# Kernel optimization log

Measured on AMD Instinct MI355X. Metric: run time of the kernel, lower is better.

Reference implementation:

```python
import jax, jax.numpy as jnp
import numpy as np

TOP_K = 8


def setup_inputs() -> dict:
    key = jax.random.key(0)
    ks = jax.random.split(key, 5)
    T, H, I, E = 4096, 2048, 1024, 64
    s = 0.02
    return {
        "x": jax.random.normal(ks[0], (T, H), jnp.float32),
        "gate_w": jax.random.normal(ks[1], (E, H), jnp.float32) * s,
        "gate_b": jax.random.normal(ks[2], (E,), jnp.float32) * s,
        "fc1_w": jax.random.normal(ks[3], (E, 2 * I, H), jnp.float32) * s,
        "fc2_w": jax.random.normal(ks[4], (E, H, I), jnp.float32) * s,
    }


def reference(x, gate_w, gate_b, fc1_w, fc2_w):
    # Router: [T, E] logits, top-k, softmax over selected logits in fp32.
    E = gate_w.shape[0]
    logits = x @ gate_w.T + gate_b
    topk_logits, topk_idx = jax.lax.top_k(logits, TOP_K)
    w = jax.nn.softmax(topk_logits.astype(jnp.float32), axis=-1).astype(x.dtype)
    # Per-token combine weight for each expert: [T, E] (0 if expert not selected).
    comb = (jax.nn.one_hot(topk_idx, E, dtype=x.dtype) * w[..., None]).sum(axis=1)
    # Scan over experts: each step is one dense GEMM-GeGLU-GEMM with masked combine.
    def body(acc, ew):
        W1, W2, c = ew  # W1 [2I, H], W2 [H, I], c [T]
        h_full = x @ W1.T                       # [T, 2I]
        h, g = jnp.split(h_full, 2, axis=-1)
        a = jax.nn.gelu(h, approximate=False) * (g + 1.0)  # custom GeGLU
        y = a @ W2.T                            # [T, H]
        return acc + c[:, None] * y, None

    out0 = jnp.zeros_like(x)
    out, _ = jax.lax.scan(body, out0, (fc1_w, fc2_w, comb.T))
    return out
```

## Files before the change

kernel.cpp:

```cpp
#include <hip/hip_runtime.h>
#include <hip/hip_bf16.h>
#include <cfloat>
#include <math.h>

#define T_TOK 4096
#define H_DIM 2048
#define E_NUM 64
#define I_DIM 1024
#define TOPK  8
#define BM    128
#define BK    64
#define MAXTILE 320

typedef __attribute__((ext_vector_type(4))) float f32x4;
typedef __attribute__((ext_vector_type(8))) short bf16x8;
typedef __attribute__((ext_vector_type(4))) int   i32x4;

__device__ __forceinline__ unsigned short f2bf(float f) {
    union { float f; unsigned int u; } v; v.f = f;
    unsigned int r = v.u + 0x7FFFu + ((v.u >> 16) & 1u);
    return (unsigned short)(r >> 16);
}
__device__ __forceinline__ unsigned int pack2(float a, float b) {
    return (unsigned int)f2bf(a) | ((unsigned int)f2bf(b) << 16);
}
__device__ __forceinline__ int cvtpk(float lo, float hi) {
    int r; asm("v_cvt_pk_bf16_f32 %0, %1, %2" : "=v"(r) : "v"(lo), "v"(hi)); return r;
}
__device__ __forceinline__ void gload16(const void* g, void* l) {
    __builtin_amdgcn_global_load_lds((const __attribute__((address_space(1))) unsigned int*)g,
                                     (__attribute__((address_space(3))) unsigned int*)l, 16, 0, 0);
}

__global__ __launch_bounds__(256)
void router_kernel(const float* __restrict__ x, const float* __restrict__ gw,
                   const float* __restrict__ gb, unsigned short* __restrict__ xb,
                   int* __restrict__ topk_idx, float* __restrict__ topk_w,
                   int* __restrict__ counts)
{
    const int t = blockIdx.x;
    const int tid = threadIdx.x;
    __shared__ float xs[H_DIM];
    __shared__ float logits[E_NUM];
    const float* xrow = x + (size_t)t * H_DIM;

    #pragma unroll
    for (int i = 0; i < 2; ++i) {
        int c = i * 1024 + tid * 4;
        f32x4 v = *(const f32x4*)(xrow + c);
        *(f32x4*)(xs + c) = v;
        uint2 pk; pk.x = pack2(v.x, v.y); pk.y = pack2(v.z, v.w);
        *(uint2*)(xb + (size_t)t * H_DIM + c) = pk;
    }
    __syncthreads();

    const int wave = tid >> 6, lane = tid & 63;
    for (int ee = 0; ee < 16; ++ee) {
        const int e = wave * 16 + ee;
        const float* g = gw + (size_t)e * H_DIM;
        float p = 0.f;
        #pragma unroll
        for (int i = 0; i < 8; ++i) {
            int c = (i * 64 + lane) * 4;
            f32x4 gv = *(const f32x4*)(g + c);
            f32x4 xv = *(const f32x4*)(xs + c);
            p += gv.x * xv.x + gv.y * xv.y + gv.z * xv.z + gv.w * xv.w;
        }
        #pragma unroll
        for (int s = 32; s > 0; s >>= 1) p += __shfl_xor(p, s, 64);
        if (lane == 0) logits[e] = p + gb[e];
    }
    __syncthreads();

    if (tid < 64) {
        float cur = logits[tid];
        float wv[TOPK]; int wi[TOPK];
        #pragma unroll
        for (int k = 0; k < TOPK; ++k) {
            float bv = cur; int bi = tid;
            #pragma unroll
            for (int s = 32; s > 0; s >>= 1) {
                float ov = __shfl_xor(bv, s, 64);
                int   oi = __shfl_xor(bi, s, 64);
                if (ov > bv || (ov == bv && oi < bi)) { bv = ov; bi = oi; }
            }
            wv[k] = bv; wi[k] = bi;
            if (tid == bi) cur = -FLT_MAX;
        }
        if (tid == 0) {
            float mx = wv[0], sum = 0.f, ex[TOPK];
            #pragma unroll
            for (int k = 0; k < TOPK; ++k) { ex[k] = expf(wv[k] - mx); sum += ex[k]; }
            #pragma unroll
            for (int k = 0; k < TOPK; ++k) {
                topk_idx[t * TOPK + k] = wi[k];
                topk_w[t * TOPK + k]   = ex[k] / sum;
                atomicAdd(&counts[wi[k]], 1);
            }
        }
    }
}

__global__ void scan_kernel(const int* __restrict__ counts, int* __restrict__ offsets,
                            int* __restrict__ cursors, int* __restrict__ tiles,
                            int* __restrict__ ntiles)
{
    if (threadIdx.x == 0) {
        int acc = 0, nt = 0;
        for (int e = 0; e < E_NUM; ++e) {
            offsets[e] = acc; cursors[e] = acc;
            int c = counts[e];
            for (int m = 0; m * BM < c; ++m) tiles[nt++] = (e << 16) | m;
            acc += c;
        }
        *ntiles = nt;
    }
}

__global__ void assign_kernel(const int* __restrict__ topk_idx, const float* __restrict__ topk_w,
                              int* __restrict__ cursors, int* __restrict__ tok_of,
                              float* __restrict__ w_of)
{
    int i = blockIdx.x * 256 + threadIdx.x;
    if (i >= T_TOK * TOPK) return;
    int e = topk_idx[i];
    int pos = atomicAdd(&cursors[e], 1);
    tok_of[pos] = i >> 3;
    w_of[pos]   = topk_w[i];
}

__global__ __launch_bounds__(256, 2)
void gemm1_kernel(const unsigned short* __restrict__ xb, const float* __restrict__ fc1,
                  const int* __restrict__ counts, const int* __restrict__ offsets,
                  const int* __restrict__ tok_of, const int* __restrict__ tiles,
                  const int* __restrict__ ntiles, unsigned short* __restrict__ a_all)
{
    const int ty = blockIdx.y;
    if (ty >= *ntiles) return;
    const int code = tiles[ty];
    const int e = code >> 16, m0 = (code & 0xffff) * BM;
    const int cnt = counts[e], off = offsets[e];
    const int n0 = blockIdx.x * BM;
    const float* W = fc1 + (size_t)e * (size_t)(2 * I_DIM) * H_DIM;

    __shared__ unsigned short sA[2][BM * BK];
    __shared__ unsigned short sB[2 * BM * BK];
    __shared__ int sTok[BM];

    const int tid = threadIdx.x;
    if (tid < BM) {
        int m = m0 + tid;
        sTok[tid] = tok_of[off + (m < cnt ? m : cnt - 1)];
    }
    __syncthreads();

    const int wid = tid >> 6, lane = tid & 63;
    const int srow = tid >> 3, sch = tid & 7;
    const int sslot = sch ^ (srow & 7);

    const unsigned short* aSrc[4];
    const float* bSrc[8];
    #pragma unroll
    for (int i = 0; i < 4; ++i) {
        int row = srow + 32 * i;
        aSrc[i] = xb + (size_t)sTok[row] * H_DIM + sslot * 8;
    }
    #pragma unroll
    for (int i = 0; i < 8; ++i) {
        int row = srow + 32 * i;
        int wrow = (row < BM) ? (n0 + row) : (I_DIM + n0 + (row - BM));
        bSrc[i] = W + (size_t)wrow * H_DIM + sch * 8;
    }

    f32x4 accH[4][4], accG[4][4];
    #pragma unroll
    for (int m = 0; m < 4; ++m)
        #pragma unroll
        for (int n = 0; n < 4; ++n) {
            accH[m][n] = (f32x4){0.f, 0.f, 0.f, 0.f};
            accG[m][n] = (f32x4){0.f, 0.f, 0.f, 0.f};
        }

    const int wm = (wid >> 1) * 64;
    const int wn = (wid & 1) * 64;
    const int fr = lane & 15;
    const int kg = lane >> 4;

    f32x4 br[16];

    auto issueB = [&](int k0) {
        #pragma unroll
        for (int i = 0; i < 8; ++i) {
            br[2 * i]     = *(const f32x4*)(bSrc[i] + k0);
            br[2 * i + 1] = *(const f32x4*)(bSrc[i] + k0 + 4);
        }
    };
    auto issueA = [&](int k0, int buf) {
        #pragma unroll
        for (int i = 0; i < 4; ++i)
            gload16(aSrc[i] + k0, &sA[buf][(32 * i + 8 * wid) * BK]);
    };
    auto writeB = [&]() {
        #pragma unroll
        for (int i = 0; i < 8; ++i) {
            int row = srow + 32 * i;
            i32x4 pk = (i32x4){cvtpk(br[2*i].x,   br[2*i].y),
                               cvtpk(br[2*i].z,   br[2*i].w),
                               cvtpk(br[2*i+1].x, br[2*i+1].y),
                               cvtpk(br[2*i+1].z, br[2*i+1].w)};
            int byte = (row * 128 + sch * 16) ^ ((row & 7) << 4);
            *(i32x4*)((char*)sB + byte) = pk;
        }
    };
    auto compute = [&](int buf) {
        #pragma unroll
        for (int kk = 0; kk < 2; ++kk) {
            bf16x8 af[4], bh[4], bg[4];
            #pragma unroll
            for (int m = 0; m < 4; ++m) {
                int row = wm + m * 16 + fr;
                af[m] = *(const bf16x8*)((const char*)sA[buf] +
                        ((row * 128 + kk * 64 + kg * 16) ^ ((row & 7) << 4)));
            }
            #pragma unroll
            for (int n = 0; n < 4; ++n) {
                int rh = wn + n * 16 + fr;
                bh[n] = *(const bf16x8*)((const char*)sB +
                        ((rh * 128 + kk * 64 + kg * 16) ^ ((rh & 7) << 4)));
                int rg = BM + rh;
                bg[n] = *(const bf16x8*)((const char*)sB +
                        ((rg * 128 + kk * 64 + kg * 16) ^ ((rg & 7) << 4)));
            }
            #pragma unroll
            for (int m = 0; m < 4; ++m)
                #pragma unroll
                for (int n = 0; n < 4; ++n) {
                    accH[m][n] = __builtin_amdgcn_mfma_f32_16x16x32_bf16(af[m], bh[n], accH[m][n], 0, 0, 0);
                    accG[m][n] = __builtin_amdgcn_mfma_f32_16x16x32_bf16(af[m], bg[n], accG[m][n], 0, 0, 0);
                }
        }
    };

    const int NT = H_DIM / BK;
    issueB(0);
    issueA(0, 0);
    __syncthreads();
    writeB();
    __syncthreads();
    int cur = 0;
    for (int t = 0; t < NT; ++t) {
        const bool more = (t + 1) < NT;
        if (more) { issueB((t + 1) * BK); issueA((t + 1) * BK, cur ^ 1); }
        compute(cur);
        __syncthreads();
        if (more) writeB();
        __syncthreads();
        cur ^= 1;
    }

    #pragma unroll
    for (int m = 0; m < 4; ++m) {
        int rbase = wm + m * 16 + kg * 4;
        #pragma unroll
        for (int r = 0; r < 4; ++r) {
            int gm = m0 + rbase + r;
            if (gm < cnt) {
                size_t rowoff = (size_t)(off + gm) * I_DIM + n0 + wn;
                #pragma unroll
                for (int n = 0; n < 4; ++n) {
                    float h = accH[m][n][r];
                    float g = accG[m][n][r];
                    float a = 0.5f * h * (1.f + erff(h * 0.70710678118f)) * (g + 1.f);
                    a_all[rowoff + n * 16 + fr] = f2bf(a);
                }
            }
        }
    }
}

__global__ __launch_bounds__(256, 2)
void gemm2_kernel(const unsigned short* __restrict__ a_all, const float* __restrict__ fc2,
                  const int* __restrict__ counts, const int* __restrict__ offsets,
                  const int* __restrict__ tok_of, const float* __restrict__ w_of,
                  const int* __restrict__ tiles, const int* __restrict__ ntiles,
                  float* __restrict__ out)
{
    const int ty = blockIdx.y;
    if (ty >= *ntiles) return;
    const int code = tiles[ty];
    const int e = code >> 16, m0 = (code & 0xffff) * BM;
    const int cnt = counts[e], off = offsets[e];
    const int n0 = blockIdx.x * BM;
    const float* W = fc2 + (size_t)e * (size_t)H_DIM * I_DIM;

    __shared__ unsigned short sA[2][BM * BK];
    __shared__ unsigned short sB[BM * BK];
    __shared__ int   sTok[BM];
    __shared__ float sWt[BM];

    const int tid = threadIdx.x;
    if (tid < BM) {
        int m = m0 + tid;
        int mm = (m < cnt) ? m : (cnt - 1);
        sTok[tid] = tok_of[off + mm];
        sWt[tid]  = w_of[off + mm];
    }

    const int wid = tid >> 6, lane = tid & 63;
    const int srow = tid >> 3, sch = tid & 7;
    const int sslot = sch ^ (srow & 7);

    const unsigned short* aSrc[4];
    const float* bSrc[4];
    #pragma unroll
    for (int i = 0; i < 4; ++i) {
        int row = srow + 32 * i;
        aSrc[i] = a_all + (size_t)(off + m0 + row) * I_DIM + sslot * 8;
        bSrc[i] = W + (size_t)(n0 + row) * I_DIM + sch * 8;
    }

    f32x4 acc[4][4];
    #pragma unroll
    for (int m = 0; m < 4; ++m)
        #pragma unroll
        for (int n = 0; n < 4; ++n) acc[m][n] = (f32x4){0.f, 0.f, 0.f, 0.f};

    const int wm = (wid >> 1) * 64;
    const int wn = (wid & 1) * 64;
    const int fr = lane & 15;
    const int kg = lane >> 4;

    f32x4 br[8];

    auto issueB = [&](int k0) {
        #pragma unroll
        for (int i = 0; i < 4; ++i) {
            br[2 * i]     = *(const f32x4*)(bSrc[i] + k0);
            br[2 * i + 1] = *(const f32x4*)(bSrc[i] + k0 + 4);
        }
    };
    auto issueA = [&](int k0, int buf) {
        #pragma unroll
        for (int i = 0; i < 4; ++i)
            gload16(aSrc[i] + k0, &sA[buf][(32 * i + 8 * wid) * BK]);
    };
    auto writeB = [&]() {
        #pragma unroll
        for (int i = 0; i < 4; ++i) {
            int row = srow + 32 * i;
            i32x4 pk = (i32x4){cvtpk(br[2*i].x,   br[2*i].y),
                               cvtpk(br[2*i].z,   br[2*i].w),
                               cvtpk(br[2*i+1].x, br[2*i+1].y),
                               cvtpk(br[2*i+1].z, br[2*i+1].w)};
            int byte = (row * 128 + sch * 16) ^ ((row & 7) << 4);
            *(i32x4*)((char*)sB + byte) = pk;
        }
    };
    auto compute = [&](int buf) {
        #pragma unroll
        for (int kk = 0; kk < 2; ++kk) {
            bf16x8 af[4], bfr[4];
            #pragma unroll
            for (int m = 0; m < 4; ++m) {
                int row = wm + m * 16 + fr;
                af[m] = *(const bf16x8*)((const char*)sA[buf] +
                        ((row * 128 + kk * 64 + kg * 16) ^ ((row & 7) << 4)));
            }
            #pragma unroll
            for (int n = 0; n < 4; ++n) {
                int row = wn + n * 16 + fr;
                bfr[n] = *(const bf16x8*)((const char*)sB +
                        ((row * 128 + kk * 64 + kg * 16) ^ ((row & 7) << 4)));
            }
            #pragma unroll
            for (int m = 0; m < 4; ++m)
                #pragma unroll
                for (int n = 0; n < 4; ++n)
                    acc[m][n] = __builtin_amdgcn_mfma_f32_16x16x32_bf16(af[m], bfr[n], acc[m][n], 0, 0, 0);
        }
    };

    const int NT = I_DIM / BK;
    issueB(0);
    issueA(0, 0);
    __syncthreads();
    writeB();
    __syncthreads();
    int cur = 0;
    for (int t = 0; t < NT; ++t) {
        const bool more = (t + 1) < NT;
        if (more) { issueB((t + 1) * BK); issueA((t + 1) * BK, cur ^ 1); }
        compute(cur);
        __syncthreads();
        if (more) writeB();
        __syncthreads();
        cur ^= 1;
    }

    #pragma unroll
    for (int m = 0; m < 4; ++m) {
        int rbase = wm + m * 16 + kg * 4;
        #pragma unroll
        for (int r = 0; r < 4; ++r) {
            int lm = rbase + r;
            int gm = m0 + lm;
            if (gm < cnt) {
                float c = sWt[lm];
                float* orow = out + (size_t)sTok[lm] * H_DIM + n0 + wn;
                #pragma unroll
                for (int n = 0; n < 4; ++n)
                    atomicAdd(&orow[n * 16 + fr], c * acc[m][n][r]);
            }
        }
    }
}

extern "C" void kernel_launch(void* const* d_in, const int* in_sizes, int n_in,
                              void* d_out, int out_size, void* d_ws, size_t ws_size,
                              hipStream_t stream)
{
    const float* x   = (const float*)d_in[0];
    const float* gw  = (const float*)d_in[1];
    const float* gb  = (const float*)d_in[2];
    const float* fc1 = (const float*)d_in[3];
    const float* fc2 = (const float*)d_in[4];
    float* out = (float*)d_out;

    char* ws = (char*)d_ws;
    size_t o = 0;
    auto alloc = [&](size_t b) { void* p = ws + o; o = (o + b + 255) & ~(size_t)255; return p; };
    unsigned short* xb     = (unsigned short*)alloc((size_t)T_TOK * H_DIM * 2);
    int*            tk_idx = (int*)  alloc((size_t)T_TOK * TOPK * 4);
    float*          tk_w   = (float*)alloc((size_t)T_TOK * TOPK * 4);
    int*            counts = (int*)  alloc(E_NUM * 4);
    int*            offs   = (int*)  alloc(E_NUM * 4);
    int*            curs   = (int*)  alloc(E_NUM * 4);
    int*            tiles  = (int*)  alloc(MAXTILE * 4);
    int*            ntiles = (int*)  alloc(4);
    int*            tok_of = (int*)  alloc((size_t)T_TOK * TOPK * 4);
    float*          w_of   = (float*)alloc((size_t)T_TOK * TOPK * 4);
    unsigned short* a_all  = (unsigned short*)alloc((size_t)(T_TOK * TOPK + BM) * I_DIM * 2);
    (void)ws_size;

    hipMemsetAsync(counts, 0, E_NUM * 4, stream);
    hipMemsetAsync(out, 0, (size_t)T_TOK * H_DIM * 4, stream);

    router_kernel<<<T_TOK, 256, 0, stream>>>(x, gw, gb, xb, tk_idx, tk_w, counts);
    scan_kernel<<<1, 64, 0, stream>>>(counts, offs, curs, tiles, ntiles);
    assign_kernel<<<(T_TOK * TOPK + 255) / 256, 256, 0, stream>>>(tk_idx, tk_w, curs, tok_of, w_of);
    gemm1_kernel<<<dim3(I_DIM / BM, MAXTILE), 256, 0, stream>>>(xb, fc1, counts, offs, tok_of,
                                                                tiles, ntiles, a_all);
    gemm2_kernel<<<dim3(H_DIM / BM, MAXTILE), 256, 0, stream>>>(a_all, fc2, counts, offs, tok_of,
                                                                w_of, tiles, ntiles, out);
}
```

Baseline: 1.149 ms.

## Use 256-row M tiles with 512-thread blocks and replace atomic scatter with combine kernel

Doubles the token-tile height to 256 rows and raises both expert GEMMs to 512 threads (8 waves), so each converted weight tile is reused across twice as many tokens and fewer tiles are launched. gemm2 now writes per-slot bf16 outputs to a workspace buffer instead of doing float atomicAdd into the output. A new combine kernel gathers each token's 8 expert rows and forms the weighted sum. This removes atomic contention and the output memset, at the cost of an extra ~128MB bf16 intermediate write/read and one more launch. Larger tiles also waste more padding rows for experts whose token counts are not multiples of 256.

```diff
diff --git a/kernel.cpp b/kernel.cpp
--- a/kernel.cpp
+++ b/kernel.cpp
@@ -8,9 +8,9 @@
 #define E_NUM 64
 #define I_DIM 1024
 #define TOPK  8
-#define BM    128
+#define BM    256
 #define BK    64
-#define MAXTILE 320
+#define MAXT  192
 
 typedef __attribute__((ext_vector_type(4))) float f32x4;
 typedef __attribute__((ext_vector_type(8))) short bf16x8;
@@ -23,6 +23,9 @@
 }
 __device__ __forceinline__ unsigned int pack2(float a, float b) {
     return (unsigned int)f2bf(a) | ((unsigned int)f2bf(b) << 16);
+}
+__device__ __forceinline__ float bf2f(unsigned short u) {
+    union { unsigned int u; float f; } v; v.u = (unsigned int)u << 16; return v.f;
 }
 __device__ __forceinline__ int cvtpk(float lo, float hi) {
     int r; asm("v_cvt_pk_bf16_f32 %0, %1, %2" : "=v"(r) : "v"(lo), "v"(hi)); return r;
@@ -119,17 +122,17 @@
 
 __global__ void assign_kernel(const int* __restrict__ topk_idx, const float* __restrict__ topk_w,
                               int* __restrict__ cursors, int* __restrict__ tok_of,
-                              float* __restrict__ w_of)
+                              int* __restrict__ pos_of)
 {
     int i = blockIdx.x * 256 + threadIdx.x;
     if (i >= T_TOK * TOPK) return;
     int e = topk_idx[i];
     int pos = atomicAdd(&cursors[e], 1);
     tok_of[pos] = i >> 3;
-    w_of[pos]   = topk_w[i];
-}
-
-__global__ __launch_bounds__(256, 2)
+    pos_of[i]   = pos;
+}
+
+__global__ __launch_bounds__(512, 1)
 void gemm1_kernel(const unsigned short* __restrict__ xb, const float* __restrict__ fc1,
                   const int* __restrict__ counts, const int* __restrict__ offsets,
                   const int* __restrict__ tok_of, const int* __restrict__ tiles,
@@ -140,11 +143,11 @@
     const int code = tiles[ty];
     const int e = code >> 16, m0 = (code & 0xffff) * BM;
     const int cnt = counts[e], off = offsets[e];
-    const int n0 = blockIdx.x * BM;
+    const int n0 = blockIdx.x * 128;
     const float* W = fc1 + (size_t)e * (size_t)(2 * I_DIM) * H_DIM;
 
     __shared__ unsigned short sA[2][BM * BK];
-    __shared__ unsigned short sB[2 * BM * BK];
+    __shared__ unsigned short sB[2 * 128 * BK];
     __shared__ int sTok[BM];
 
     const int tid = threadIdx.x;
@@ -159,16 +162,12 @@
     const int sslot = sch ^ (srow & 7);
 
     const unsigned short* aSrc[4];
-    const float* bSrc[8];
+    const float* bSrc[4];
     #pragma unroll
     for (int i = 0; i < 4; ++i) {
-        int row = srow + 32 * i;
+        int row = srow + 64 * i;
         aSrc[i] = xb + (size_t)sTok[row] * H_DIM + sslot * 8;
-    }
-    #pragma unroll
-    for (int i = 0; i < 8; ++i) {
-        int row = srow + 32 * i;
-        int wrow = (row < BM) ? (n0 + row) : (I_DIM + n0 + (row - BM));
+        int wrow = (row < 128) ? (n0 + row) : (I_DIM + n0 + (row - 128));
         bSrc[i] = W + (size_t)wrow * H_DIM + sch * 8;
     }
 
@@ -182,15 +181,15 @@
         }
 
     const int wm = (wid >> 1) * 64;
-    const int wn = (wid & 1) * 64;
+    const int wnp = (wid & 1) * 64;
     const int fr = lane & 15;
     const int kg = lane >> 4;
 
-    f32x4 br[16];
+    f32x4 br[8];
 
     auto issueB = [&](int k0) {
         #pragma unroll
-        for (int i = 0; i < 8; ++i) {
+        for (int i = 0; i < 4; ++i) {
             br[2 * i]     = *(const f32x4*)(bSrc[i] + k0);
             br[2 * i + 1] = *(const f32x4*)(bSrc[i] + k0 + 4);
         }
@@ -198,12 +197,12 @@
     auto issueA = [&](int k0, int buf) {
         #pragma unroll
         for (int i = 0; i < 4; ++i)
-            gload16(aSrc[i] + k0, &sA[buf][(32 * i + 8 * wid) * BK]);
+            gload16(aSrc[i] + k0, &sA[buf][(64 * i + 8 * wid) * BK]);
     };
     auto writeB = [&]() {
         #pragma unroll
-        for (int i = 0; i < 8; ++i) {
-            int row = srow + 32 * i;
+        for (int i = 0; i < 4; ++i) {
+            int row = srow + 64 * i;
             i32x4 pk = (i32x4){cvtpk(br[2*i].x,   br[2*i].y),
                                cvtpk(br[2*i].z,   br[2*i].w),
                                cvtpk(br[2*i+1].x, br[2*i+1].y),
@@ -224,10 +223,10 @@
             }
             #pragma unroll
             for (int n = 0; n < 4; ++n) {
-                int rh = wn + n * 16 + fr;
+                int rh = wnp + n * 16 + fr;
                 bh[n] = *(const bf16x8*)((const char*)sB +
                         ((rh * 128 + kk * 64 + kg * 16) ^ ((rh & 7) << 4)));
-                int rg = BM + rh;
+                int rg = 128 + rh;
                 bg[n] = *(const bf16x8*)((const char*)sB +
                         ((rg * 128 + kk * 64 + kg * 16) ^ ((rg & 7) << 4)));
             }
@@ -265,7 +264,7 @@
         for (int r = 0; r < 4; ++r) {
             int gm = m0 + rbase + r;
             if (gm < cnt) {
-                size_t rowoff = (size_t)(off + gm) * I_DIM + n0 + wn;
+                size_t rowoff = (size_t)(off + gm) * I_DIM + n0 + wnp;
                 #pragma unroll
                 for (int n = 0; n < 4; ++n) {
                     float h = accH[m][n][r];
@@ -278,44 +277,38 @@
     }
 }
 
-__global__ __launch_bounds__(256, 2)
+__global__ __launch_bounds__(512, 1)
 void gemm2_kernel(const unsigned short* __restrict__ a_all, const float* __restrict__ fc2,
                   const int* __restrict__ counts, const int* __restrict__ offsets,
-                  const int* __restrict__ tok_of, const float* __restrict__ w_of,
                   const int* __restrict__ tiles, const int* __restrict__ ntiles,
-                  float* __restrict__ out)
+                  unsigned short* __restrict__ y)
 {
     const int ty = blockIdx.y;
     if (ty >= *ntiles) return;
     const int code = tiles[ty];
     const int e = code >> 16, m0 = (code & 0xffff) * BM;
     const int cnt = counts[e], off = offsets[e];
-    const int n0 = blockIdx.x * BM;
+    const int n0 = blockIdx.x * 128;
     const float* W = fc2 + (size_t)e * (size_t)H_DIM * I_DIM;
 
     __shared__ unsigned short sA[2][BM * BK];
-    __shared__ unsigned short sB[BM * BK];
-    __shared__ int   sTok[BM];
-    __shared__ float sWt[BM];
+    __shared__ unsigned short sB[128 * BK];
 
     const int tid = threadIdx.x;
-    if (tid < BM) {
-        int m = m0 + tid;
-        int mm = (m < cnt) ? m : (cnt - 1);
-        sTok[tid] = tok_of[off + mm];
-        sWt[tid]  = w_of[off + mm];
-    }
-
     const int wid = tid >> 6, lane = tid & 63;
     const int srow = tid >> 3, sch = tid & 7;
     const int sslot = sch ^ (srow & 7);
 
     const unsigned short* aSrc[4];
-    const float* bSrc[4];
+    const float* bSrc[2];
     #pragma unroll
     for (int i = 0; i < 4; ++i) {
-        int row = srow + 32 * i;
+        int row = srow + 64 * i;
         aSrc[i] = a_all + (size_t)(off + m0 + row) * I_DIM + sslot * 8;
+    }
+    #pragma unroll
+    for (int i = 0; i < 2; ++i) {
+        int row = srow + 64 * i;
         bSrc[i] = W + (size_t)(n0 + row) * I_DIM + sch * 8;
     }
 
@@ -330,11 +323,11 @@
     const int fr = lane & 15;
     const int kg = lane >> 4;
 
-    f32x4 br[8];
+    f32x4 br[4];
 
     auto issueB = [&](int k0) {
         #pragma unroll
-        for (int i = 0; i < 4; ++i) {
+        for (int i = 0; i < 2; ++i) {
             br[2 * i]     = *(const f32x4*)(bSrc[i] + k0);
             br[2 * i + 1] = *(const f32x4*)(bSrc[i] + k0 + 4);
         }
@@ -342,12 +335,12 @@
     auto issueA = [&](int k0, int buf) {
         #pragma unroll
         for (int i = 0; i < 4; ++i)
-            gload16(aSrc[i] + k0, &sA[buf][(32 * i + 8 * wid) * BK]);
+            gload16(aSrc[i] + k0, &sA[buf][(64 * i + 8 * wid) * BK]);
     };
     auto writeB = [&]() {
         #pragma unroll
-        for (int i = 0; i < 4; ++i) {
-            int row = srow + 32 * i;
+        for (int i = 0; i < 2; ++i) {
+            int row = srow + 64 * i;
             i32x4 pk = (i32x4){cvtpk(br[2*i].x,   br[2*i].y),
                                cvtpk(br[2*i].z,   br[2*i].w),
                                cvtpk(br[2*i+1].x, br[2*i+1].y),
@@ -402,17 +395,46 @@
         int rbase = wm + m * 16 + kg * 4;
         #pragma unroll
         for (int r = 0; r < 4; ++r) {
-            int lm = rbase + r;
-            int gm = m0 + lm;
+            int gm = m0 + rbase + r;
             if (gm < cnt) {
-                float c = sWt[lm];
-                float* orow = out + (size_t)sTok[lm] * H_DIM + n0 + wn;
+                size_t rowoff = (size_t)(off + gm) * H_DIM + n0 + wn;
                 #pragma unroll
                 for (int n = 0; n < 4; ++n)
-                    atomicAdd(&orow[n * 16 + fr], c * acc[m][n][r]);
-            }
-        }
-    }
+                    y[rowoff + n * 16 + fr] = f2bf(acc[m][n][r]);
+            }
+        }
+    }
+}
+
+__global__ __launch_bounds__(256)
+void combine_kernel(const unsigned short* __restrict__ y, const int* __restrict__ pos_of,
+                    const float* __restrict__ topk_w, float* __restrict__ out)
+{
+    const int t = blockIdx.x;
+    const int tid = threadIdx.x;
+    __shared__ int   sp[TOPK];
+    __shared__ float sw[TOPK];
+    if (tid < TOPK) {
+        sp[tid] = pos_of[t * TOPK + tid];
+        sw[tid] = topk_w[t * TOPK + tid];
+    }
+    __syncthreads();
+
+    const int c0 = tid * 8;
+    float acc[8];
+    #pragma unroll
+    for (int j = 0; j < 8; ++j) acc[j] = 0.f;
+    #pragma unroll
+    for (int k = 0; k < TOPK; ++k) {
+        const float w = sw[k];
+        i32x4 v = *(const i32x4*)(y + (size_t)sp[k] * H_DIM + c0);
+        const unsigned short* u = (const unsigned short*)&v;
+        #pragma unroll
+        for (int j = 0; j < 8; ++j) acc[j] += w * bf2f(u[j]);
+    }
+    float* orow = out + (size_t)t * H_DIM + c0;
+    *(f32x4*)orow       = (f32x4){acc[0], acc[1], acc[2], acc[3]};
+    *(f32x4*)(orow + 4) = (f32x4){acc[4], acc[5], acc[6], acc[7]};
 }
 
 extern "C" void kernel_launch(void* const* d_in, const int* in_sizes, int n_in,
@@ -435,21 +457,22 @@
     int*            counts = (int*)  alloc(E_NUM * 4);
     int*            offs   = (int*)  alloc(E_NUM * 4);
     int*            curs   = (int*)  alloc(E_NUM * 4);
-    int*            tiles  = (int*)  alloc(MAXTILE * 4);
+    int*            tiles  = (int*)  alloc(MAXT * 4);
     int*            ntiles = (int*)  alloc(4);
     int*            tok_of = (int*)  alloc((size_t)T_TOK * TOPK * 4);
-    float*          w_of   = (float*)alloc((size_t)T_TOK * TOPK * 4);
+    int*            pos_of = (int*)  alloc((size_t)T_TOK * TOPK * 4);
     unsigned short* a_all  = (unsigned short*)alloc((size_t)(T_TOK * TOPK + BM) * I_DIM * 2);
+    unsigned short* yb     = (unsigned short*)alloc((size_t)T_TOK * TOPK * H_DIM * 2);
     (void)ws_size;
 
     hipMemsetAsync(counts, 0, E_NUM * 4, stream);
-    hipMemsetAsync(out, 0, (size_t)T_TOK * H_DIM * 4, stream);
 
     router_kernel<<<T_TOK, 256, 0, stream>>>(x, gw, gb, xb, tk_idx, tk_w, counts);
     scan_kernel<<<1, 64, 0, stream>>>(counts, offs, curs, tiles, ntiles);
-    assign_kernel<<<(T_TOK * TOPK + 255) / 256, 256, 0, stream>>>(tk_idx, tk_w, curs, tok_of, w_of);
-    gemm1_kernel<<<dim3(I_DIM / BM, MAXTILE), 256, 0, stream>>>(xb, fc1, counts, offs, tok_of,
-                                                                tiles, ntiles, a_all);
-    gemm2_kernel<<<dim3(H_DIM / BM, MAXTILE), 256, 0, stream>>>(a_all, fc2, counts, offs, tok_of,
-                                                                w_of, tiles, ntiles, out);
-}
+    assign_kernel<<<(T_TOK * TOPK + 255) / 256, 256, 0, stream>>>(tk_idx, tk_w, curs, tok_of, pos_of);
+    gemm1_kernel<<<dim3(I_DIM / 128, MAXT), 512, 0, stream>>>(xb, fc1, counts, offs, tok_of,
+                                                              tiles, ntiles, a_all);
+    gemm2_kernel<<<dim3(H_DIM / 128, MAXT), 512, 0, stream>>>(a_all, fc2, counts, offs,
+                                                              tiles, ntiles, yb);
+    combine_kernel<<<T_TOK, 256, 0, stream>>>(yb, pos_of, tk_w, out);
+}
```

Result: slower. 1.261 ms (+9.8%).
